# Optimization experiments

Hardware: AMD Instinct MI355X
Metric: run time of the kernel (lower is better)

Reference implementation:

```python
import jax, jax.numpy as jnp
import numpy as np

IN_C = 256
OUT_C = 256
HID = IN_C * 2
N_POINTS = 262144
N_NODES = 8192
B = 16
MAX_NODES = 512
EPS = 1e-5


def _mlp(h, w1, b1, g1, be1, w2, b2):
    # PyG MLP([C, 2C, out], norm='layer_norm'): lin -> layernorm -> relu -> (dropout, eval=identity) -> lin
    h = h @ w1 + b1
    mu = jnp.mean(h, axis=-1, keepdims=True)
    var = jnp.var(h, axis=-1, keepdims=True)
    h = (h - mu) * jax.lax.rsqrt(var + EPS) * g1 + be1
    h = jax.nn.relu(h)
    return h @ w2 + b2


def setup_inputs() -> dict:
    key = jax.random.key(0)
    ks = jax.random.split(key, 16)
    x = jax.random.normal(ks[0], (N_POINTS, IN_C), dtype=jnp.float32)
    f_point_batches = jnp.sort(jax.random.randint(ks[1], (N_POINTS,), 0, N_NODES)).astype(jnp.int32)
    # equal-sized graphs (16 graphs x 512 nodes), sorted as torch.split/pad_sequence assume
    g_node_batches = jnp.repeat(jnp.arange(B, dtype=jnp.int32), MAX_NODES)
    s = 1.0 / np.sqrt(IN_C)
    s2 = 1.0 / np.sqrt(HID)
    def lin(k, fan_in, shape, scale):
        return jax.random.uniform(k, shape, jnp.float32, -scale, scale)
    params = {}
    for i, name in enumerate(['Wq', 'Wk']):
        base = 2 + i * 6
        params[f'{name}_w1'] = lin(ks[base + 0], IN_C, (IN_C, HID), s)
        params[f'{name}_b1'] = lin(ks[base + 1], IN_C, (HID,), s)
        params[f'{name}_g1'] = jnp.ones((HID,), jnp.float32)
        params[f'{name}_be1'] = jnp.zeros((HID,), jnp.float32)
        params[f'{name}_w2'] = lin(ks[base + 2], HID, (HID, OUT_C), s2)
        params[f'{name}_b2'] = lin(ks[base + 3], HID, (OUT_C,), s2)
    return dict(x=x, f_point_batches=f_point_batches, g_node_batches=g_node_batches,
                num_graphs=B, max_nodes=MAX_NODES, **params)


def reference(x, f_point_batches, g_node_batches, num_graphs, max_nodes,
              Wq_w1, Wq_b1, Wq_g1, Wq_be1, Wq_w2, Wq_b2,
              Wk_w1, Wk_b1, Wk_g1, Wk_be1, Wk_w2, Wk_b2):
    n_nodes = g_node_batches.shape[0]
    C = x.shape[1]
    # scatter_mean over points -> per-node feature means [n_nodes, C]
    sums = jax.ops.segment_sum(x, f_point_batches, num_segments=n_nodes)
    cnt = jax.ops.segment_sum(jnp.ones((x.shape[0],), x.dtype), f_point_batches, num_segments=n_nodes)
    mean = sums / jnp.maximum(cnt, 1.0)[:, None]
    # ragged split by graph + pad_sequence -> [B, max_nodes, C]
    starts = jnp.searchsorted(g_node_batches, jnp.arange(num_graphs, dtype=g_node_batches.dtype))
    pos = jnp.arange(n_nodes) - starts[g_node_batches]
    padded = jnp.zeros((num_graphs, max_nodes, C), x.dtype).at[g_node_batches, pos].set(mean, mode='drop')
    q = _mlp(padded, Wq_w1, Wq_b1, Wq_g1, Wq_be1, Wq_w2, Wq_b2)  # [B, MAXN, out]
    k = _mlp(padded, Wk_w1, Wk_b1, Wk_g1, Wk_be1, Wk_w2, Wk_b2)
    return jnp.einsum('bnd,bmd->bnm', q, k)  # bmm(q, k^T)
```

## Files before the change

kernel.cpp:

```cpp
#include <hip/hip_runtime.h>
#include <hip/hip_bf16.h>

#define N_POINTS 262144
#define N_NODES  8192
#define IN_C     256
#define HID      512
#define OUT_C    256
#define NB       16
#define MAXN     512
#define EPSV     1e-5f
#define NPB      32

typedef __attribute__((ext_vector_type(8))) short short8;
typedef __attribute__((ext_vector_type(4))) float f32x4;
typedef __attribute__((ext_vector_type(4))) float f4v;
#define MFMA16(a, b, c) __builtin_amdgcn_mfma_f32_16x16x32_bf16((a), (b), (c), 0, 0, 0)


__global__ __launch_bounds__(256) void prelude_k(
    const int* __restrict__ fpb, int* __restrict__ starts,
    const float* __restrict__ W1q, const float* __restrict__ W1k,
    const float* __restrict__ W2q, const float* __restrict__ W2k,
    __hip_bfloat16* __restrict__ P1q, __hip_bfloat16* __restrict__ P1k,
    __hip_bfloat16* __restrict__ P2q, __hip_bfloat16* __restrict__ P2k)
{
  if (blockIdx.x < 1024) {
    const int i = blockIdx.x * 256 + threadIdx.x;
    const int cur = fpb[i];
    const int prev = (i == 0) ? -1 : fpb[i - 1];
    for (int n = prev + 1; n <= cur; ++n) starts[n] = i;
    if (i == N_POINTS - 1)
      for (int n = cur + 1; n <= N_NODES; ++n) starts[n] = N_POINTS;
    return;
  }
  const int bid = blockIdx.x - 1024;
  const int sel = bid >> 6;
  const float* W; __hip_bfloat16* P; int N;
  switch (sel) {
    case 0:  W = W1q; P = P1q; N = HID;   break;
    case 1:  W = W1k; P = P1k; N = HID;   break;
    case 2:  W = W2q; P = P2q; N = OUT_C; break;
    default: W = W2k; P = P2k; N = OUT_C; break;
  }
  const int idx = (bid & 63) * 256 + threadIdx.x;
  const int NF = N >> 4;
  const int lane = idx & 63;
  const int nf = (idx >> 6) % NF;
  const int ks = idx / (64 * NF);
  const int k0 = ks * 32 + (lane >> 4) * 8;
  const int n  = nf * 16 + (lane & 15);
  __hip_bfloat16 tmp[8];
  #pragma unroll
  for (int j = 0; j < 8; ++j) tmp[j] = __float2bfloat16(W[(size_t)(k0 + j) * N + n]);
  *(uint4*)(P + (size_t)idx * 8) = *(uint4*)tmp;
}

__device__ __forceinline__ void accum_rows(
    const float* __restrict__ x, int lo, int hi, int l,
    f4v& a0, f4v& a1, f4v& a2, f4v& a3)
{
  int r = lo;
  for (; r + 4 <= hi; r += 4) {
    f4v v0 = *(const f4v*)(x + (size_t)(r + 0) * IN_C + l * 4);
    f4v v1 = *(const f4v*)(x + (size_t)(r + 1) * IN_C + l * 4);
    f4v v2 = *(const f4v*)(x + (size_t)(r + 2) * IN_C + l * 4);
    f4v v3 = *(const f4v*)(x + (size_t)(r + 3) * IN_C + l * 4);
    a0 += v0; a1 += v1; a2 += v2; a3 += v3;
  }
  for (; r < hi; ++r)
    a0 += *(const f4v*)(x + (size_t)r * IN_C + l * 4);
}

__global__ __launch_bounds__(1024, 4) void fused_mlp_k(
    const float* __restrict__ x, const int* __restrict__ starts,
    const __hip_bfloat16* __restrict__ P1q, const __hip_bfloat16* __restrict__ P2q,
    const float* __restrict__ b1q, const float* __restrict__ g1q,
    const float* __restrict__ be1q, const float* __restrict__ b2q,
    const __hip_bfloat16* __restrict__ P1k, const __hip_bfloat16* __restrict__ P2k,
    const float* __restrict__ b1k, const float* __restrict__ g1k,
    const float* __restrict__ be1k, const float* __restrict__ b2k,
    __hip_bfloat16* __restrict__ qo, __hip_bfloat16* __restrict__ ko)
{
  const int n0 = blockIdx.x * NPB;
  const int t = threadIdx.x;
  const int w = t >> 6, l = t & 63, lg = l >> 4, lm = l & 15;
  const int h = w >> 3;
  const int c = w & 7;

  const __hip_bfloat16* P1 = h ? P1k : P1q;
  const __hip_bfloat16* P2 = h ? P2k : P2q;
  const float* b1  = h ? b1k  : b1q;
  const float* g1  = h ? g1k  : g1q;
  const float* be1 = h ? be1k : be1q;
  const float* b2  = h ? b2k  : b2q;
  __hip_bfloat16* out = h ? ko : qo;

  __shared__ __hip_bfloat16 As[NPB * 264];
  __shared__ __hip_bfloat16 Hs[2][NPB * 520];
  __shared__ float lnp[16][NPB][2];
  __hip_bfloat16* Hsh = Hs[h];

  #pragma unroll
  for (int i = 0; i < 2; ++i) {
    const int nl = w * 2 + i;
    const int node = n0 + nl;
    const int s_ = starts[node], e_ = starts[node + 1];
    f4v a0 = (f4v)0.f, a1 = (f4v)0.f, a2 = (f4v)0.f, a3 = (f4v)0.f;
    accum_rows(x, s_, e_, l, a0, a1, a2, a3);
    a0 += a1 + a2 + a3;
    const int cnt = e_ - s_;
    const float inv = cnt > 0 ? 1.0f / (float)cnt : 0.0f;
    __hip_bfloat16 o[4];
    o[0] = __float2bfloat16(a0.x * inv);
    o[1] = __float2bfloat16(a0.y * inv);
    o[2] = __float2bfloat16(a0.z * inv);
    o[3] = __float2bfloat16(a0.w * inv);
    *(uint2*)(As + nl * 264 + l * 4) = *(uint2*)o;
  }
  __syncthreads();

  f32x4 acc1[2][4];
  #pragma unroll
  for (int mi = 0; mi < 2; ++mi)
    #pragma unroll
    for (int nj = 0; nj < 4; ++nj)
      #pragma unroll
      for (int r = 0; r < 4; ++r) acc1[mi][nj][r] = 0.f;

  for (int ks = 0; ks < 8; ++ks) {
    short8 a0 = *(const short8*)(As + lm * 264 + ks * 32 + lg * 8);
    short8 a1 = *(const short8*)(As + (16 + lm) * 264 + ks * 32 + lg * 8);
    const __hip_bfloat16* bp = P1 + ((size_t)(ks * 32 + c * 4) * 64 + l) * 8;
    #pragma unroll
    for (int nj = 0; nj < 4; ++nj) {
      short8 b = *(const short8*)(bp + (size_t)nj * 512);
      acc1[0][nj] = MFMA16(a0, b, acc1[0][nj]);
      acc1[1][nj] = MFMA16(a1, b, acc1[1][nj]);
    }
  }

  float b1v[4], g1v[4], e1v[4];
  #pragma unroll
  for (int nj = 0; nj < 4; ++nj) {
    const int col = c * 64 + nj * 16 + lm;
    b1v[nj] = b1[col]; g1v[nj] = g1[col]; e1v[nj] = be1[col];
  }
  #pragma unroll
  for (int mi = 0; mi < 2; ++mi)
    #pragma unroll
    for (int nj = 0; nj < 4; ++nj)
      #pragma unroll
      for (int r = 0; r < 4; ++r) acc1[mi][nj][r] += b1v[nj];

  #pragma unroll
  for (int mi = 0; mi < 2; ++mi)
    #pragma unroll
    for (int r = 0; r < 4; ++r) {
      float s = 0.f, q = 0.f;
      #pragma unroll
      for (int nj = 0; nj < 4; ++nj) {
        const float v = acc1[mi][nj][r];
        s += v; q += v * v;
      }
      #pragma unroll
      for (int off = 1; off < 16; off <<= 1) {
        s += __shfl_xor(s, off);
        q += __shfl_xor(q, off);
      }
      if (lm == 0) {
        const int row = mi * 16 + lg * 4 + r;
        lnp[w][row][0] = s;
        lnp[w][row][1] = q;
      }
    }
  __syncthreads();

  #pragma unroll
  for (int mi = 0; mi < 2; ++mi)
    #pragma unroll
    for (int r = 0; r < 4; ++r) {
      const int row = mi * 16 + lg * 4 + r;
      float S = 0.f, Q = 0.f;
      #pragma unroll
      for (int w2 = 0; w2 < 8; ++w2) {
        S += lnp[h * 8 + w2][row][0];
        Q += lnp[h * 8 + w2][row][1];
      }
      const float mu = S * (1.0f / HID);
      const float rs = rsqrtf(Q * (1.0f / HID) - mu * mu + EPSV);
      #pragma unroll
      for (int nj = 0; nj < 4; ++nj) {
        const float y = (acc1[mi][nj][r] - mu) * rs * g1v[nj] + e1v[nj];
        Hsh[row * 520 + c * 64 + nj * 16 + lm] = __float2bfloat16(fmaxf(y, 0.f));
      }
    }
  __syncthreads();

  f32x4 acc2[2][2];
  #pragma unroll
  for (int mi = 0; mi < 2; ++mi)
    #pragma unroll
    for (int nj = 0; nj < 2; ++nj)
      #pragma unroll
      for (int r = 0; r < 4; ++r) acc2[mi][nj][r] = 0.f;

  for (int ks = 0; ks < 16; ++ks) {
    short8 a0 = *(const short8*)(Hsh + lm * 520 + ks * 32 + lg * 8);
    short8 a1 = *(const short8*)(Hsh + (16 + lm) * 520 + ks * 32 + lg * 8);
    const __hip_bfloat16* bp = P2 + ((size_t)(ks * 16 + c * 2) * 64 + l) * 8;
    #pragma unroll
    for (int nj = 0; nj < 2; ++nj) {
      short8 b = *(const short8*)(bp + (size_t)nj * 512);
      acc2[0][nj] = MFMA16(a0, b, acc2[0][nj]);
      acc2[1][nj] = MFMA16(a1, b, acc2[1][nj]);
    }
  }

  float b2v[2];
  #pragma unroll
  for (int nj = 0; nj < 2; ++nj) b2v[nj] = b2[c * 32 + nj * 16 + lm];
  #pragma unroll
  for (int mi = 0; mi < 2; ++mi)
    #pragma unroll
    for (int nj = 0; nj < 2; ++nj)
      #pragma unroll
      for (int r = 0; r < 4; ++r) {
        const int row = n0 + mi * 16 + lg * 4 + r;
        const int col = c * 32 + nj * 16 + lm;
        out[(size_t)row * OUT_C + col] = __float2bfloat16(acc2[mi][nj][r] + b2v[nj]);
      }
}

__global__ __launch_bounds__(256, 4) void bmm_k(
    const __hip_bfloat16* __restrict__ q, const __hip_bfloat16* __restrict__ k,
    float* __restrict__ out)
{
  const int b  = blockIdx.z;
  const int n0 = blockIdx.x * 64;
  const int m0 = blockIdx.y * 64;
  const int t = threadIdx.x;
  const int w = t >> 6, l = t & 63, lg = l >> 4, lm = l & 15;

  const __hip_bfloat16* qb = q + ((size_t)b * MAXN + n0 + w * 16) * OUT_C;
  const __hip_bfloat16* kb = k + ((size_t)b * MAXN + m0) * OUT_C;

  f32x4 acc[4];
  #pragma unroll
  for (int nj = 0; nj < 4; ++nj)
    #pragma unroll
    for (int r = 0; r < 4; ++r) acc[nj][r] = 0.f;

  for (int ks = 0; ks < 8; ++ks) {
    short8 a = *(const short8*)(qb + (size_t)lm * OUT_C + ks * 32 + lg * 8);
    #pragma unroll
    for (int nj = 0; nj < 4; ++nj) {
      short8 bb = *(const short8*)(kb + (size_t)(nj * 16 + lm) * OUT_C + ks * 32 + lg * 8);
      acc[nj] = MFMA16(a, bb, acc[nj]);
    }
  }

  #pragma unroll
  for (int nj = 0; nj < 4; ++nj)
    #pragma unroll
    for (int r = 0; r < 4; ++r) {
      const int nrow = n0 + w * 16 + lg * 4 + r;
      const int mcol = m0 + nj * 16 + lm;
      out[((size_t)b * MAXN + nrow) * MAXN + mcol] = acc[nj][r];
    }
}

extern "C" void kernel_launch(void* const* d_in, const int* in_sizes, int n_in,
                              void* d_out, int out_size, void* d_ws, size_t ws_size,
                              hipStream_t stream)
{
  const float* x   = (const float*)d_in[0];
  const int*   fpb = (const int*)d_in[1];
  const float* Wq_w1  = (const float*)d_in[5];
  const float* Wq_b1  = (const float*)d_in[6];
  const float* Wq_g1  = (const float*)d_in[7];
  const float* Wq_be1 = (const float*)d_in[8];
  const float* Wq_w2  = (const float*)d_in[9];
  const float* Wq_b2  = (const float*)d_in[10];
  const float* Wk_w1  = (const float*)d_in[11];
  const float* Wk_b1  = (const float*)d_in[12];
  const float* Wk_g1  = (const float*)d_in[13];
  const float* Wk_be1 = (const float*)d_in[14];
  const float* Wk_w2  = (const float*)d_in[15];
  const float* Wk_b2  = (const float*)d_in[16];

  __hip_bfloat16* ws = (__hip_bfloat16*)d_ws;
  __hip_bfloat16* P1q  = ws;
  __hip_bfloat16* P1k  = P1q + 131072;
  __hip_bfloat16* P2q  = P1k + 131072;
  __hip_bfloat16* P2k  = P2q + 131072;
  __hip_bfloat16* qo   = P2k + 131072;
  __hip_bfloat16* ko   = qo + 2097152;
  int* starts = (int*)(ko + 2097152);
  float* out = (float*)d_out;

  prelude_k<<<1280, 256, 0, stream>>>(fpb, starts,
      Wq_w1, Wk_w1, Wq_w2, Wk_w2, P1q, P1k, P2q, P2k);
  fused_mlp_k<<<N_NODES / NPB, 1024, 0, stream>>>(
      x, starts, P1q, P2q, Wq_b1, Wq_g1, Wq_be1, Wq_b2,
      P1k, P2k, Wk_b1, Wk_g1, Wk_be1, Wk_b2, qo, ko);
  bmm_k<<<dim3(8, 8, NB), 256, 0, stream>>>(qo, ko, out);
}
```

Baseline: 87.69 us.

## Balance scatter-mean point reduction across waves with shared-memory atomic accumulation

Before, each wave summed the points of two fixed nodes, so waves with larger nodes set the pace of the block. Now the block's whole contiguous point range is split evenly across the 16 waves. Each wave binary-searches for its starting node, accumulates partial sums per node segment, and adds them into a float buffer in shared memory (reusing the hidden-activation buffer) with atomics. A final pass normalizes by count and writes bf16 to As. This adds shared atomics, an extra barrier and a zeroing pass, but is meant to remove load imbalance in the memory-bound gather.

```diff
diff --git a/kernel.cpp b/kernel.cpp
--- a/kernel.cpp
+++ b/kernel.cpp
@@ -55,22 +55,6 @@
   *(uint4*)(P + (size_t)idx * 8) = *(uint4*)tmp;
 }
 
-__device__ __forceinline__ void accum_rows(
-    const float* __restrict__ x, int lo, int hi, int l,
-    f4v& a0, f4v& a1, f4v& a2, f4v& a3)
-{
-  int r = lo;
-  for (; r + 4 <= hi; r += 4) {
-    f4v v0 = *(const f4v*)(x + (size_t)(r + 0) * IN_C + l * 4);
-    f4v v1 = *(const f4v*)(x + (size_t)(r + 1) * IN_C + l * 4);
-    f4v v2 = *(const f4v*)(x + (size_t)(r + 2) * IN_C + l * 4);
-    f4v v3 = *(const f4v*)(x + (size_t)(r + 3) * IN_C + l * 4);
-    a0 += v0; a1 += v1; a2 += v2; a3 += v3;
-  }
-  for (; r < hi; ++r)
-    a0 += *(const f4v*)(x + (size_t)r * IN_C + l * 4);
-}
-
 __global__ __launch_bounds__(1024, 4) void fused_mlp_k(
     const float* __restrict__ x, const int* __restrict__ starts,
     const __hip_bfloat16* __restrict__ P1q, const __hip_bfloat16* __restrict__ P2q,
@@ -96,26 +80,66 @@
   __hip_bfloat16* out = h ? ko : qo;
 
   __shared__ __hip_bfloat16 As[NPB * 264];
-  __shared__ __hip_bfloat16 Hs[2][NPB * 520];
+  __shared__ __hip_bfloat16 HsBuf[2 * NPB * 520];
   __shared__ float lnp[16][NPB][2];
-  __hip_bfloat16* Hsh = Hs[h];
-
-  #pragma unroll
-  for (int i = 0; i < 2; ++i) {
-    const int nl = w * 2 + i;
-    const int node = n0 + nl;
-    const int s_ = starts[node], e_ = starts[node + 1];
-    f4v a0 = (f4v)0.f, a1 = (f4v)0.f, a2 = (f4v)0.f, a3 = (f4v)0.f;
-    accum_rows(x, s_, e_, l, a0, a1, a2, a3);
-    a0 += a1 + a2 + a3;
-    const int cnt = e_ - s_;
+  __shared__ int startsL[NPB + 1];
+  float* sums = (float*)HsBuf;
+  __hip_bfloat16* Hsh = HsBuf + (size_t)h * (NPB * 520);
+
+  if (t <= NPB) startsL[t] = starts[n0 + t];
+  {
+    f4v z = (f4v)0.f;
+    *(f4v*)(sums + t * 8)     = z;
+    *(f4v*)(sums + t * 8 + 4) = z;
+  }
+  __syncthreads();
+
+  {
+    const int S = startsL[0], E = startsL[NPB];
+    const int R = E - S;
+    const int chunk = (R + 15) >> 4;
+    int r = S + w * chunk;
+    const int rend = min(r + chunk, E);
+    if (r < rend) {
+      int lo = 0, hi = NPB - 1;
+      while (lo < hi) { int m = (lo + hi + 1) >> 1; if (startsL[m] <= r) lo = m; else hi = m - 1; }
+      int node = lo;
+      int nb = startsL[node + 1];
+      while (r < rend) {
+        const int stop = min(rend, nb);
+        f4v a0 = (f4v)0.f, a1 = (f4v)0.f, a2 = (f4v)0.f, a3 = (f4v)0.f;
+        for (; r + 4 <= stop; r += 4) {
+          f4v v0 = *(const f4v*)(x + (size_t)(r + 0) * IN_C + l * 4);
+          f4v v1 = *(const f4v*)(x + (size_t)(r + 1) * IN_C + l * 4);
+          f4v v2 = *(const f4v*)(x + (size_t)(r + 2) * IN_C + l * 4);
+          f4v v3 = *(const f4v*)(x + (size_t)(r + 3) * IN_C + l * 4);
+          a0 += v0; a1 += v1; a2 += v2; a3 += v3;
+        }
+        for (; r < stop; ++r)
+          a0 += *(const f4v*)(x + (size_t)r * IN_C + l * 4);
+        a0 += a1 + a2 + a3;
+        float* sp = sums + node * IN_C + l * 4;
+        atomicAdd(sp + 0, a0.x);
+        atomicAdd(sp + 1, a0.y);
+        atomicAdd(sp + 2, a0.z);
+        atomicAdd(sp + 3, a0.w);
+        if (r >= rend) break;
+        ++node; nb = startsL[node + 1];
+      }
+    }
+  }
+  __syncthreads();
+
+  {
+    const int nl = t >> 5;
+    const int c8 = (t & 31) * 8;
+    const int cnt = startsL[nl + 1] - startsL[nl];
     const float inv = cnt > 0 ? 1.0f / (float)cnt : 0.0f;
-    __hip_bfloat16 o[4];
-    o[0] = __float2bfloat16(a0.x * inv);
-    o[1] = __float2bfloat16(a0.y * inv);
-    o[2] = __float2bfloat16(a0.z * inv);
-    o[3] = __float2bfloat16(a0.w * inv);
-    *(uint2*)(As + nl * 264 + l * 4) = *(uint2*)o;
+    const float* sp = sums + nl * IN_C + c8;
+    __hip_bfloat16 o[8];
+    #pragma unroll
+    for (int j = 0; j < 8; ++j) o[j] = __float2bfloat16(sp[j] * inv);
+    *(uint4*)(As + nl * 264 + c8) = *(uint4*)o;
   }
   __syncthreads();
 
```

New measurement: 91.20 us. 4.0% more time.

## Split scatter-mean into its own kernel and prefetch weight fragments in MLP

Applied to the files above, without the earlier changes.

Moves the per-node mean reduction out of the fused MLP kernel into a separate scatter_mean kernel with small 256-thread blocks, and stores the node means as bf16 in workspace. The MLP kernel then loads means with wide vector copies. Both MLP GEMM k-loops now double-buffer the weight fragments in registers, loading step ks+1 while computing step ks. The split is meant to spread the bandwidth-heavy 256 MB read of x across more, smaller blocks instead of tying it to the large MLP blocks. The cost is an extra kernel launch, a round trip of the means through global memory, and higher register pressure in the MLP kernel.

```diff
diff --git a/kernel.cpp b/kernel.cpp
--- a/kernel.cpp
+++ b/kernel.cpp
@@ -71,8 +71,28 @@
     a0 += *(const f4v*)(x + (size_t)r * IN_C + l * 4);
 }
 
-__global__ __launch_bounds__(1024, 4) void fused_mlp_k(
+__global__ __launch_bounds__(256) void scatter_mean_k(
     const float* __restrict__ x, const int* __restrict__ starts,
+    __hip_bfloat16* __restrict__ mean)
+{
+  const int node = blockIdx.x * 4 + (threadIdx.x >> 6);
+  const int l = threadIdx.x & 63;
+  const int s_ = starts[node], e_ = starts[node + 1];
+  f4v a0 = (f4v)0.f, a1 = (f4v)0.f, a2 = (f4v)0.f, a3 = (f4v)0.f;
+  accum_rows(x, s_, e_, l, a0, a1, a2, a3);
+  a0 += a1 + a2 + a3;
+  const int cnt = e_ - s_;
+  const float inv = cnt > 0 ? 1.0f / (float)cnt : 0.0f;
+  __hip_bfloat16 o[4];
+  o[0] = __float2bfloat16(a0.x * inv);
+  o[1] = __float2bfloat16(a0.y * inv);
+  o[2] = __float2bfloat16(a0.z * inv);
+  o[3] = __float2bfloat16(a0.w * inv);
+  *(uint2*)(mean + (size_t)node * IN_C + l * 4) = *(uint2*)o;
+}
+
+__global__ __launch_bounds__(1024, 4) void mlp_k(
+    const __hip_bfloat16* __restrict__ mean,
     const __hip_bfloat16* __restrict__ P1q, const __hip_bfloat16* __restrict__ P2q,
     const float* __restrict__ b1q, const float* __restrict__ g1q,
     const float* __restrict__ be1q, const float* __restrict__ b2q,
@@ -100,22 +120,10 @@
   __shared__ float lnp[16][NPB][2];
   __hip_bfloat16* Hsh = Hs[h];
 
-  #pragma unroll
-  for (int i = 0; i < 2; ++i) {
-    const int nl = w * 2 + i;
-    const int node = n0 + nl;
-    const int s_ = starts[node], e_ = starts[node + 1];
-    f4v a0 = (f4v)0.f, a1 = (f4v)0.f, a2 = (f4v)0.f, a3 = (f4v)0.f;
-    accum_rows(x, s_, e_, l, a0, a1, a2, a3);
-    a0 += a1 + a2 + a3;
-    const int cnt = e_ - s_;
-    const float inv = cnt > 0 ? 1.0f / (float)cnt : 0.0f;
-    __hip_bfloat16 o[4];
-    o[0] = __float2bfloat16(a0.x * inv);
-    o[1] = __float2bfloat16(a0.y * inv);
-    o[2] = __float2bfloat16(a0.z * inv);
-    o[3] = __float2bfloat16(a0.w * inv);
-    *(uint2*)(As + nl * 264 + l * 4) = *(uint2*)o;
+  {
+    const int nl = t >> 5, c8 = (t & 31) * 8;
+    uint4 v = *(const uint4*)(mean + (size_t)(n0 + nl) * IN_C + c8);
+    *(uint4*)(As + nl * 264 + c8) = v;
   }
   __syncthreads();
 
@@ -127,16 +135,27 @@
       #pragma unroll
       for (int r = 0; r < 4; ++r) acc1[mi][nj][r] = 0.f;
 
+  short8 bcur[4], bnxt[4];
+  {
+    const __hip_bfloat16* bp = P1 + ((size_t)(c * 4) * 64 + l) * 8;
+    #pragma unroll
+    for (int nj = 0; nj < 4; ++nj) bcur[nj] = *(const short8*)(bp + (size_t)nj * 512);
+  }
   for (int ks = 0; ks < 8; ++ks) {
+    if (ks < 7) {
+      const __hip_bfloat16* bp = P1 + ((size_t)((ks + 1) * 32 + c * 4) * 64 + l) * 8;
+      #pragma unroll
+      for (int nj = 0; nj < 4; ++nj) bnxt[nj] = *(const short8*)(bp + (size_t)nj * 512);
+    }
     short8 a0 = *(const short8*)(As + lm * 264 + ks * 32 + lg * 8);
     short8 a1 = *(const short8*)(As + (16 + lm) * 264 + ks * 32 + lg * 8);
-    const __hip_bfloat16* bp = P1 + ((size_t)(ks * 32 + c * 4) * 64 + l) * 8;
     #pragma unroll
     for (int nj = 0; nj < 4; ++nj) {
-      short8 b = *(const short8*)(bp + (size_t)nj * 512);
-      acc1[0][nj] = MFMA16(a0, b, acc1[0][nj]);
-      acc1[1][nj] = MFMA16(a1, b, acc1[1][nj]);
-    }
+      acc1[0][nj] = MFMA16(a0, bcur[nj], acc1[0][nj]);
+      acc1[1][nj] = MFMA16(a1, bcur[nj], acc1[1][nj]);
+    }
+    #pragma unroll
+    for (int nj = 0; nj < 4; ++nj) bcur[nj] = bnxt[nj];
   }
 
   float b1v[4], g1v[4], e1v[4];
@@ -204,16 +223,27 @@
       #pragma unroll
       for (int r = 0; r < 4; ++r) acc2[mi][nj][r] = 0.f;
 
+  short8 b2cur[2], b2nxt[2];
+  {
+    const __hip_bfloat16* bp = P2 + ((size_t)(c * 2) * 64 + l) * 8;
+    #pragma unroll
+    for (int nj = 0; nj < 2; ++nj) b2cur[nj] = *(const short8*)(bp + (size_t)nj * 512);
+  }
   for (int ks = 0; ks < 16; ++ks) {
+    if (ks < 15) {
+      const __hip_bfloat16* bp = P2 + ((size_t)((ks + 1) * 16 + c * 2) * 64 + l) * 8;
+      #pragma unroll
+      for (int nj = 0; nj < 2; ++nj) b2nxt[nj] = *(const short8*)(bp + (size_t)nj * 512);
+    }
     short8 a0 = *(const short8*)(Hsh + lm * 520 + ks * 32 + lg * 8);
     short8 a1 = *(const short8*)(Hsh + (16 + lm) * 520 + ks * 32 + lg * 8);
-    const __hip_bfloat16* bp = P2 + ((size_t)(ks * 16 + c * 2) * 64 + l) * 8;
     #pragma unroll
     for (int nj = 0; nj < 2; ++nj) {
-      short8 b = *(const short8*)(bp + (size_t)nj * 512);
-      acc2[0][nj] = MFMA16(a0, b, acc2[0][nj]);
-      acc2[1][nj] = MFMA16(a1, b, acc2[1][nj]);
-    }
+      acc2[0][nj] = MFMA16(a0, b2cur[nj], acc2[0][nj]);
+      acc2[1][nj] = MFMA16(a1, b2cur[nj], acc2[1][nj]);
+    }
+    #pragma unroll
+    for (int nj = 0; nj < 2; ++nj) b2cur[nj] = b2nxt[nj];
   }
 
   float b2v[2];
@@ -293,15 +323,17 @@
   __hip_bfloat16* P1k  = P1q + 131072;
   __hip_bfloat16* P2q  = P1k + 131072;
   __hip_bfloat16* P2k  = P2q + 131072;
-  __hip_bfloat16* qo   = P2k + 131072;
+  __hip_bfloat16* mean = P2k + 131072;
+  __hip_bfloat16* qo   = mean + 2097152;
   __hip_bfloat16* ko   = qo + 2097152;
   int* starts = (int*)(ko + 2097152);
   float* out = (float*)d_out;
 
   prelude_k<<<1280, 256, 0, stream>>>(fpb, starts,
       Wq_w1, Wk_w1, Wq_w2, Wk_w2, P1q, P1k, P2q, P2k);
-  fused_mlp_k<<<N_NODES / NPB, 1024, 0, stream>>>(
-      x, starts, P1q, P2q, Wq_b1, Wq_g1, Wq_be1, Wq_b2,
+  scatter_mean_k<<<N_NODES / 4, 256, 0, stream>>>(x, starts, mean);
+  mlp_k<<<N_NODES / NPB, 1024, 0, stream>>>(
+      mean, P1q, P2q, Wq_b1, Wq_g1, Wq_be1, Wq_b2,
       P1k, P2k, Wk_b1, Wk_g1, Wk_be1, Wk_b2, qo, ko);
   bmm_k<<<dim3(8, 8, NB), 256, 0, stream>>>(qo, ko, out);
 }
```

Measured after the change: 94.75 us. 8.0% more time.
